# Kernel optimization log

Measured on AMD Instinct MI355X. Metric: run time of the kernel, lower is better.

## Reference

```python
import jax, jax.numpy as jnp
import numpy as np

B, C, H, W = 2, 512, 64, 64
G = 32          # GroupNorm groups
EPS = 1e-6


def setup_inputs() -> dict:
    key = jax.random.key(0)
    ks = jax.random.split(key, 10)
    s = 1.0 / np.sqrt(C)
    return {
        "x": jax.random.normal(ks[0], (B, C, H, W), dtype=jnp.float32),
        "gn_w": jnp.ones((C,), jnp.float32),
        "gn_b": jnp.zeros((C,), jnp.float32),
        "wq": jax.random.normal(ks[1], (C, C), jnp.float32) * s,
        "bq": jnp.zeros((C,), jnp.float32),
        "wk": jax.random.normal(ks[2], (C, C), jnp.float32) * s,
        "bk": jnp.zeros((C,), jnp.float32),
        "wv": jax.random.normal(ks[3], (C, C), jnp.float32) * s,
        "bv": jnp.zeros((C,), jnp.float32),
        "wo": jax.random.normal(ks[4], (C, C), jnp.float32) * s,
        "bo": jnp.zeros((C,), jnp.float32),
    }


def reference(x, gn_w, gn_b, wq, bq, wk, bk, wv, bv, wo, bo):
    b, c, h, w = x.shape
    n = h * w
    # GroupNorm(32, eps=1e-6, affine)
    xg = x.reshape(b, G, c // G, h, w)
    mu = xg.mean(axis=(2, 3, 4), keepdims=True)
    var = ((xg - mu) ** 2).mean(axis=(2, 3, 4), keepdims=True)
    hn = ((xg - mu) * jax.lax.rsqrt(var + EPS)).reshape(b, c, h, w)
    hn = hn * gn_w[None, :, None, None] + gn_b[None, :, None, None]
    # 1x1 convs == per-pixel linear over channels; tokens: b n c
    hf = hn.reshape(b, c, n)
    q = jnp.einsum('oc,bcn->bno', wq, hf) + bq  # [b, n, c]
    k = jnp.einsum('oc,bcn->bno', wk, hf) + bk
    v = jnp.einsum('oc,bcn->bno', wv, hf) + bv
    scale = jnp.asarray(c, x.dtype) ** -0.5
    att = jax.nn.softmax(jnp.einsum('bic,bjc->bij', q, k) * scale, axis=-1)
    o = jnp.einsum('bij,bjc->bic', att, v)      # [b, n, c]
    out = jnp.einsum('oc,bnc->bno', wo, o) + bo # proj_out
    return x + out.transpose(0, 2, 1).reshape(b, c, h, w)
```

## Files before the change

kernel.cpp:

```cpp
#include <hip/hip_runtime.h>
#include <hip/hip_bf16.h>


typedef float f32x4 __attribute__((ext_vector_type(4)));
typedef __bf16 bf16x8 __attribute__((ext_vector_type(8)));

typedef const __attribute__((address_space(1))) unsigned char* gas_p;
typedef __attribute__((address_space(3))) unsigned char* las_p;

__device__ __forceinline__ void gload_lds16(const void* g, void* l) {
  __builtin_amdgcn_global_load_lds((gas_p)g, (las_p)l, 16, 0, 0);
}

__global__ __launch_bounds__(256) void prelude_k(
    const float* __restrict__ wq, const float* __restrict__ wk,
    const float* __restrict__ wv, const float* __restrict__ wo,
    __hip_bfloat16* __restrict__ wqkb, __hip_bfloat16* __restrict__ wvb,
    __hip_bfloat16* __restrict__ wob, const float* __restrict__ bq,
    const float* __restrict__ bk, float* __restrict__ bqk,
    const float* __restrict__ x, float* __restrict__ stats) {
  int bid = blockIdx.x;
  if (bid < 4096) {
    const float* src;
    __hip_bfloat16* dst;
    if (bid < 1024)      { src = wq; dst = wqkb; }
    else if (bid < 2048) { src = wk; dst = wqkb + 262144; }
    else if (bid < 3072) { src = wv; dst = wvb; }
    else                 { src = wo; dst = wob; }
    int i = (bid & 1023) * 256 + threadIdx.x;
    dst[i] = __float2bfloat16(src[i]);
    return;
  }
  if (bid < 4160) {
    int bg = bid - 4096;
    const float4* p = (const float4*)(x + (size_t)bg * 65536);
    float s = 0.f, s2 = 0.f;
    for (int i = threadIdx.x; i < 16384; i += 256) {
      float4 v = p[i];
      s  += v.x + v.y + v.z + v.w;
      s2 += v.x * v.x + v.y * v.y + v.z * v.z + v.w * v.w;
    }
#pragma unroll
    for (int off = 32; off > 0; off >>= 1) {
      s  += __shfl_xor(s, off);
      s2 += __shfl_xor(s2, off);
    }
    __shared__ float rs[4], rs2[4];
    int wid = threadIdx.x >> 6, lane = threadIdx.x & 63;
    if (lane == 0) { rs[wid] = s; rs2[wid] = s2; }
    __syncthreads();
    if (threadIdx.x == 0) {
      float S  = rs[0] + rs[1] + rs[2] + rs[3];
      float S2 = rs2[0] + rs2[1] + rs2[2] + rs2[3];
      float mean = S * (1.f / 65536.f);
      float var  = S2 * (1.f / 65536.f) - mean * mean;
      stats[bg * 2]     = mean;
      stats[bg * 2 + 1] = rsqrtf(var + 1e-6f);
    }
    return;
  }
  for (int j = threadIdx.x; j < 1024; j += 256)
    bqk[j] = (j < 512) ? bq[j] : bk[j - 512];
}

__global__ __launch_bounds__(256) void gn_apply_k(const float* __restrict__ x,
                                                  const float* __restrict__ stats,
                                                  const float* __restrict__ gw,
                                                  const float* __restrict__ gb,
                                                  __hip_bfloat16* __restrict__ hf) {
  int c0 = blockIdx.x * 64, n0 = blockIdx.y * 64, b = blockIdx.z;
  __shared__ float tile[64][65];
  int tid = threadIdx.x;
  int cl = tid >> 2, q = tid & 3;
  int c = c0 + cl;
  float mean = stats[(b * 32 + (c >> 4)) * 2];
  float rstd = stats[(b * 32 + (c >> 4)) * 2 + 1];
  float sc = rstd * gw[c];
  float sh = gb[c] - mean * sc;
  const float* xr = x + ((size_t)(b * 512 + c0 + cl)) * 4096 + n0 + q * 16;
#pragma unroll
  for (int j = 0; j < 4; j++) {
    float4 v = *(const float4*)(xr + 4 * j);
    int n = q * 16 + 4 * j;
    tile[cl][n]     = v.x * sc + sh;
    tile[cl][n + 1] = v.y * sc + sh;
    tile[cl][n + 2] = v.z * sc + sh;
    tile[cl][n + 3] = v.w * sc + sh;
  }
  __syncthreads();
  int nl = tid >> 2, ch = q * 16;
  bf16x8 o0, o1;
#pragma unroll
  for (int l = 0; l < 8; l++) {
    o0[l] = (__bf16)tile[ch + l][nl];
    o1[l] = (__bf16)tile[ch + 8 + l][nl];
  }
  __hip_bfloat16* op = hf + ((size_t)(b * 4096 + n0 + nl)) * 512 + c0 + ch;
  *(uint4*)op = *(uint4*)&o0;
  *(uint4*)(op + 8) = *(uint4*)&o1;
}

__global__ __launch_bounds__(256, 4) void qkv_k(
    const __hip_bfloat16* __restrict__ hf, const __hip_bfloat16* __restrict__ wqk,
    const __hip_bfloat16* __restrict__ wv, const float* __restrict__ bqk,
    const float* __restrict__ bv, __hip_bfloat16* __restrict__ qk,
    __hip_bfloat16* __restrict__ vT) {
  bool isV = blockIdx.x >= 8;
  int m0 = isV ? (blockIdx.x - 8) * 128 : blockIdx.y * 128;
  int n0 = isV ? blockIdx.y * 128 : blockIdx.x * 128;
  const __hip_bfloat16* A  = isV ? wv : hf;
  const __hip_bfloat16* Bm = isV ? hf : wqk;

  __shared__ __align__(16) unsigned char smem[34816];
  __hip_bfloat16* As  = (__hip_bfloat16*)smem;
  __hip_bfloat16* Bs  = As + 8192;
  __hip_bfloat16* epi = (__hip_bfloat16*)smem;

  int tid  = threadIdx.x;
  int wvx  = tid >> 6, lane = tid & 63;
  int wr   = (wvx >> 1) * 64, wc = (wvx & 1) * 64;
  int quad = lane >> 4, l16 = lane & 15;

  int srow = wvx * 32 + (lane >> 2);
  int scol = (lane & 3) * 8;
  const __hip_bfloat16* gA0 = A  + (size_t)(m0 + srow) * 512 + scol;
  const __hip_bfloat16* gA1 = gA0 + (size_t)16 * 512;
  const __hip_bfloat16* gB0 = Bm + (size_t)(n0 + srow) * 512 + scol;
  const __hip_bfloat16* gB1 = gB0 + (size_t)16 * 512;

  auto stage = [&](int kk, int bsel) {
    int lb = bsel * 4096 + wvx * 1024;
    gload_lds16(gA0 + kk, &As[lb]);
    gload_lds16(gA1 + kk, &As[lb + 512]);
    gload_lds16(gB0 + kk, &Bs[lb]);
    gload_lds16(gB1 + kk, &Bs[lb + 512]);
  };

  f32x4 acc[4][4] = {};
  stage(0, 0);
  for (int kt = 0; kt < 16; kt++) {
    __syncthreads();
    if (kt + 1 < 16) stage((kt + 1) << 5, (kt + 1) & 1);
    const __hip_bfloat16* Ab = &As[(kt & 1) * 4096];
    const __hip_bfloat16* Bb = &Bs[(kt & 1) * 4096];
    bf16x8 af[4], bfr[4];
#pragma unroll
    for (int i = 0; i < 4; i++)
      af[i] = *(const bf16x8*)&Ab[(wr + i * 16 + l16) * 32 + quad * 8];
#pragma unroll
    for (int j = 0; j < 4; j++)
      bfr[j] = *(const bf16x8*)&Bb[(wc + j * 16 + l16) * 32 + quad * 8];
#pragma unroll
    for (int i = 0; i < 4; i++)
#pragma unroll
      for (int j = 0; j < 4; j++)
        acc[i][j] = __builtin_amdgcn_mfma_f32_16x16x32_bf16(af[i], bfr[j],
                                                            acc[i][j], 0, 0, 0);
  }

  float bj[4], bm[4][4];
  if (!isV) {
#pragma unroll
    for (int j = 0; j < 4; j++) bj[j] = bqk[n0 + wc + j * 16 + l16];
  } else {
#pragma unroll
    for (int i = 0; i < 4; i++)
#pragma unroll
      for (int r = 0; r < 4; r++)
        bm[i][r] = bv[m0 + wr + i * 16 + quad * 4 + r];
  }
  __syncthreads();
#pragma unroll
  for (int i = 0; i < 4; i++)
#pragma unroll
    for (int j = 0; j < 4; j++)
#pragma unroll
      for (int r = 0; r < 4; r++) {
        int ml = wr + i * 16 + quad * 4 + r;
        int nl = wc + j * 16 + l16;
        float v = acc[i][j][r] + (isV ? bm[i][r] : bj[j]);
        epi[ml * 136 + nl] = __float2bfloat16(v);
      }
  __syncthreads();
  int mr = tid >> 1, h = tid & 1;
  const __hip_bfloat16* rowp = &epi[mr * 136 + h * 64];
  if (!isV) {
    __hip_bfloat16* o = qk + (size_t)(m0 + mr) * 1024 + n0 + h * 64;
#pragma unroll
    for (int c = 0; c < 8; c++)
      *(uint4*)(o + c * 8) = *(const uint4*)(rowp + c * 8);
  } else {
    int b = (n0 + h * 64) >> 12, t = (n0 + h * 64) & 4095;
    __hip_bfloat16* o = vT + ((size_t)(b * 512 + m0 + mr)) * 4096 + t;
#pragma unroll
    for (int c = 0; c < 8; c++)
      *(uint4*)(o + c * 8) = *(const uint4*)(rowp + c * 8);
  }
}

__global__ __launch_bounds__(256, 4) void qkexp_k(
    const __hip_bfloat16* __restrict__ A, const __hip_bfloat16* __restrict__ Bm,
    __hip_bfloat16* __restrict__ Cout, float* __restrict__ psums) {
  int bx = blockIdx.x, by = blockIdx.y, bb = blockIdx.z;
  const float scale = 0.044194173824159216f;
  A  += (size_t)bb * 4096 * 1024;
  Bm += (size_t)bb * 4096 * 1024 + 512;
  size_t cbase = (size_t)bb * 4096 * 4096;
  int m0 = by * 128, n0 = bx * 128;

  __shared__ __align__(16) unsigned char smem[33792];
  __hip_bfloat16* As  = (__hip_bfloat16*)smem;
  __hip_bfloat16* Bs  = As + 8192;
  float* psum2 = (float*)(smem + 32768);

  int tid  = threadIdx.x;
  int wv   = tid >> 6, lane = tid & 63;
  int wr   = (wv >> 1) * 64, wc = (wv & 1) * 64;
  int quad = lane >> 4, l16 = lane & 15;

  int srow = wv * 32 + (lane >> 2);
  int scol = (lane & 3) * 8;
  const __hip_bfloat16* gA0 = A  + (size_t)(m0 + srow) * 1024 + scol;
  const __hip_bfloat16* gA1 = gA0 + (size_t)16 * 1024;
  const __hip_bfloat16* gB0 = Bm + (size_t)(n0 + srow) * 1024 + scol;
  const __hip_bfloat16* gB1 = gB0 + (size_t)16 * 1024;

  auto stage = [&](int kk, int bsel) {
    int lb = bsel * 4096 + wv * 1024;
    gload_lds16(gA0 + kk, &As[lb]);
    gload_lds16(gA1 + kk, &As[lb + 512]);
    gload_lds16(gB0 + kk, &Bs[lb]);
    gload_lds16(gB1 + kk, &Bs[lb + 512]);
  };

  f32x4 acc[4][4] = {};
  stage(0, 0);
  for (int kt = 0; kt < 16; kt++) {
    __syncthreads();
    if (kt + 1 < 16) stage((kt + 1) << 5, (kt + 1) & 1);
    const __hip_bfloat16* Ab = &As[(kt & 1) * 4096];
    const __hip_bfloat16* Bb = &Bs[(kt & 1) * 4096];
    bf16x8 af[4], bfr[4];
#pragma unroll
    for (int i = 0; i < 4; i++)
      af[i] = *(const bf16x8*)&Ab[(wr + i * 16 + l16) * 32 + quad * 8];
#pragma unroll
    for (int j = 0; j < 4; j++)
      bfr[j] = *(const bf16x8*)&Bb[(wc + j * 16 + l16) * 32 + quad * 8];
#pragma unroll
    for (int i = 0; i < 4; i++)
#pragma unroll
      for (int j = 0; j < 4; j++)
        acc[i][j] = __builtin_amdgcn_mfma_f32_16x16x32_bf16(af[i], bfr[j],
                                                            acc[i][j], 0, 0, 0);
  }

  float s[4][4];
#pragma unroll
  for (int i = 0; i < 4; i++)
#pragma unroll
    for (int r = 0; r < 4; r++) s[i][r] = 0.f;
#pragma unroll
  for (int i = 0; i < 4; i++)
#pragma unroll
    for (int j = 0; j < 4; j++)
#pragma unroll
      for (int r = 0; r < 4; r++) {
        int m = m0 + wr + i * 16 + quad * 4 + r;
        int n = n0 + wc + j * 16 + l16;
        float v = __expf(acc[i][j][r] * scale);
        Cout[cbase + (size_t)m * 4096 + n] = __float2bfloat16(v);
        s[i][r] += v;
      }
#pragma unroll
  for (int off = 1; off < 16; off <<= 1)
#pragma unroll
    for (int i = 0; i < 4; i++)
#pragma unroll
      for (int r = 0; r < 4; r++) s[i][r] += __shfl_xor(s[i][r], off);
  if (l16 == 0) {
#pragma unroll
    for (int i = 0; i < 4; i++)
#pragma unroll
      for (int r = 0; r < 4; r++)
        psum2[(wv & 1) * 128 + wr + i * 16 + quad * 4 + r] = s[i][r];
  }
  __syncthreads();
  if (tid < 128)
    psums[(size_t)bx * 8192 + bb * 4096 + m0 + tid] =
        psum2[tid] + psum2[128 + tid];
}

__global__ __launch_bounds__(256, 2) void pv_k(
    const __hip_bfloat16* __restrict__ P, const __hip_bfloat16* __restrict__ vT,
    __hip_bfloat16* __restrict__ part) {
  int f = blockIdx.x;
  int xcd = f & 7, s = f >> 3;
  int bx = s & 3;
  int g = xcd + 8 * (s >> 2);
  int by = g & 31, bz = g >> 5;
  int bb = bz >> 1, ks = bz & 1;
  const __hip_bfloat16* A = P  + (size_t)bb * 4096 * 4096 + (size_t)ks * 2048;
  const __hip_bfloat16* B = vT + (size_t)bb * 512 * 4096 + (size_t)ks * 2048;
  size_t cbase = (size_t)bz * 4096 * 512;
  int m0 = by * 128, n0 = bx * 128;

  __shared__ __align__(16) unsigned char smem[65536];
  __hip_bfloat16* As  = (__hip_bfloat16*)smem;
  __hip_bfloat16* Bs  = (__hip_bfloat16*)(smem + 32768);
  __hip_bfloat16* epi = (__hip_bfloat16*)smem;

  int tid = threadIdx.x, wv = tid >> 6, lane = tid & 63;
  int wr = (wv >> 1) * 64, wc = (wv & 1) * 64;
  int quad = lane >> 4, l16 = lane & 15;

  int srow = wv * 32 + (lane >> 3);
  int scol = ((lane & 7) ^ (lane >> 3)) * 8;
  const __hip_bfloat16* gA = A + (size_t)(m0 + srow) * 4096 + scol;
  const __hip_bfloat16* gB = B + (size_t)(n0 + srow) * 4096 + scol;

  auto stage = [&](int kk, int bsel) {
    __hip_bfloat16* la = &As[bsel * 8192 + wv * 2048];
    __hip_bfloat16* lb = &Bs[bsel * 8192 + wv * 2048];
#pragma unroll
    for (int c = 0; c < 4; c++) {
      gload_lds16(gA + kk + (size_t)(c * 8) * 4096, la + c * 512);
      gload_lds16(gB + kk + (size_t)(c * 8) * 4096, lb + c * 512);
    }
  };

  f32x4 acc[4][4] = {};
  stage(0, 0);
  for (int kt = 0; kt < 32; kt++) {
    __syncthreads();
    if (kt + 1 < 32) stage((kt + 1) << 6, (kt + 1) & 1);
    const __hip_bfloat16* Ab = &As[(kt & 1) * 8192];
    const __hip_bfloat16* Bb = &Bs[(kt & 1) * 8192];
#pragma unroll
    for (int ksub = 0; ksub < 2; ksub++) {
      bf16x8 af[4], bfr[4];
#pragma unroll
      for (int i = 0; i < 4; i++) {
        int r = wr + i * 16 + l16;
        af[i] = *(const bf16x8*)&Ab[r * 64 + ((ksub * 4 + quad) ^ (r & 7)) * 8];
      }
#pragma unroll
      for (int j = 0; j < 4; j++) {
        int r = wc + j * 16 + l16;
        bfr[j] = *(const bf16x8*)&Bb[r * 64 + ((ksub * 4 + quad) ^ (r & 7)) * 8];
      }
#pragma unroll
      for (int i = 0; i < 4; i++)
#pragma unroll
        for (int j = 0; j < 4; j++)
          acc[i][j] = __builtin_amdgcn_mfma_f32_16x16x32_bf16(af[i], bfr[j],
                                                              acc[i][j], 0, 0, 0);
    }
  }

  __syncthreads();
#pragma unroll
  for (int i = 0; i < 4; i++)
#pragma unroll
    for (int j = 0; j < 4; j++)
#pragma unroll
      for (int r = 0; r < 4; r++)
        epi[(wr + i * 16 + quad * 4 + r) * 136 + wc + j * 16 + l16] =
            __float2bfloat16(acc[i][j][r]);
  __syncthreads();
  int mr = tid >> 1, h = tid & 1;
  const __hip_bfloat16* rowp = &epi[mr * 136 + h * 64];
  __hip_bfloat16* o = part + cbase + (size_t)(m0 + mr) * 512 + n0 + h * 64;
#pragma unroll
  for (int c = 0; c < 8; c++)
    *(uint4*)(o + c * 8) = *(const uint4*)(rowp + c * 8);
}

__global__ __launch_bounds__(256) void reduce_k(
    const __hip_bfloat16* __restrict__ part, const float* __restrict__ psums,
    __hip_bfloat16* __restrict__ obuf) {
  size_t i8 = (size_t)blockIdx.x * 256 + threadIdx.x;
  size_t perb = (size_t)4096 * 512 / 8;
  size_t b = i8 / perb, r = i8 - b * perb;
  int t = (int)(r >> 6);
  int lane = threadIdx.x & 63;
  float ps = psums[(size_t)(lane & 31) * 8192 + b * 4096 + t];
#pragma unroll
  for (int off = 1; off < 32; off <<= 1) ps += __shfl_xor(ps, off);
  float inv = 1.f / ps;
  float acc[8] = {};
#pragma unroll
  for (int ks = 0; ks < 2; ks++) {
    bf16x8 v = ((const bf16x8*)part)[(b * 2 + ks) * perb + r];
#pragma unroll
    for (int l = 0; l < 8; l++) acc[l] += (float)v[l];
  }
  bf16x8 o;
#pragma unroll
  for (int l = 0; l < 8; l++) o[l] = (__bf16)(acc[l] * inv);
  ((bf16x8*)obuf)[b * perb + r] = o;
}

__global__ __launch_bounds__(256, 2) void oproj_k(
    const __hip_bfloat16* __restrict__ Wo, const __hip_bfloat16* __restrict__ O,
    float* __restrict__ out, const float* __restrict__ bias,
    const float* __restrict__ resid) {
  int m0 = blockIdx.y * 64, n0 = blockIdx.x * 128, bb = blockIdx.z;
  O += (size_t)bb * 4096 * 512;
  size_t cbase = (size_t)bb * 512 * 4096;

  __shared__ __align__(16) unsigned char smem[24576];
  __hip_bfloat16* As  = (__hip_bfloat16*)smem;
  __hip_bfloat16* Bs  = As + 4096;
  __hip_bfloat16* epi = (__hip_bfloat16*)smem;

  int tid = threadIdx.x, wv = tid >> 6, lane = tid & 63;
  int wr = (wv >> 1) * 32, wc = (wv & 1) * 64;
  int quad = lane >> 4, l16 = lane & 15;

  int lr = lane >> 2, scol = (lane & 3) * 8;
  const __hip_bfloat16* gA  = Wo + (size_t)(m0 + wv * 16 + lr) * 512 + scol;
  const __hip_bfloat16* gB0 = O  + (size_t)(n0 + wv * 32 + lr) * 512 + scol;
  const __hip_bfloat16* gB1 = gB0 + (size_t)16 * 512;

  auto stage = [&](int kk, int bsel) {
    gload_lds16(gA + kk, &As[bsel * 2048 + wv * 512]);
    gload_lds16(gB0 + kk, &Bs[bsel * 4096 + wv * 1024]);
    gload_lds16(gB1 + kk, &Bs[bsel * 4096 + wv * 1024 + 512]);
  };

  f32x4 acc[2][4] = {};
  stage(0, 0);
  for (int kt = 0; kt < 16; kt++) {
    __syncthreads();
    if (kt + 1 < 16) stage((kt + 1) << 5, (kt + 1) & 1);
    const __hip_bfloat16* Ab = &As[(kt & 1) * 2048];
    const __hip_bfloat16* Bb = &Bs[(kt & 1) * 4096];
    bf16x8 af[2], bfr[4];
#pragma unroll
    for (int i = 0; i < 2; i++)
      af[i] = *(const bf16x8*)&Ab[(wr + i * 16 + l16) * 32 + quad * 8];
#pragma unroll
    for (int j = 0; j < 4; j++)
      bfr[j] = *(const bf16x8*)&Bb[(wc + j * 16 + l16) * 32 + quad * 8];
#pragma unroll
    for (int i = 0; i < 2; i++)
#pragma unroll
      for (int j = 0; j < 4; j++)
        acc[i][j] = __builtin_amdgcn_mfma_f32_16x16x32_bf16(af[i], bfr[j],
                                                            acc[i][j], 0, 0, 0);
  }

  float pre[2][4];
#pragma unroll
  for (int i = 0; i < 2; i++)
#pragma unroll
    for (int r = 0; r < 4; r++)
      pre[i][r] = bias[m0 + wr + i * 16 + quad * 4 + r];
  __syncthreads();
#pragma unroll
  for (int i = 0; i < 2; i++)
#pragma unroll
    for (int j = 0; j < 4; j++)
#pragma unroll
      for (int r = 0; r < 4; r++)
        epi[(wr + i * 16 + quad * 4 + r) * 136 + wc + j * 16 + l16] =
            __float2bfloat16(acc[i][j][r] + pre[i][r]);
  __syncthreads();
  int mr = tid >> 2, seg = tid & 3;
  const __hip_bfloat16* rowp = &epi[mr * 136 + seg * 32];
  size_t obase = cbase + (size_t)(m0 + mr) * 4096 + n0 + seg * 32;
#pragma unroll
  for (int c = 0; c < 4; c++) {
    bf16x8 val = *(const bf16x8*)(rowp + c * 8);
    size_t idx = obase + c * 8;
    float4 r0 = *(const float4*)&resid[idx];
    float4 r1 = *(const float4*)&resid[idx + 4];
    float4 o0, o1;
    o0.x = r0.x + (float)val[0]; o0.y = r0.y + (float)val[1];
    o0.z = r0.z + (float)val[2]; o0.w = r0.w + (float)val[3];
    o1.x = r1.x + (float)val[4]; o1.y = r1.y + (float)val[5];
    o1.z = r1.z + (float)val[6]; o1.w = r1.w + (float)val[7];
    *(float4*)&out[idx] = o0;
    *(float4*)&out[idx + 4] = o1;
  }
}

extern "C" void kernel_launch(void* const* d_in, const int* in_sizes, int n_in,
                              void* d_out, int out_size, void* d_ws,
                              size_t ws_size, hipStream_t stream) {
  const float* xp  = (const float*)d_in[0];
  const float* gwp = (const float*)d_in[1];
  const float* gbp = (const float*)d_in[2];
  const float* wqp = (const float*)d_in[3];
  const float* bqp = (const float*)d_in[4];
  const float* wkp = (const float*)d_in[5];
  const float* bkp = (const float*)d_in[6];
  const float* wvp = (const float*)d_in[7];
  const float* bvp = (const float*)d_in[8];
  const float* wop = (const float*)d_in[9];
  const float* bop = (const float*)d_in[10];
  float* outp = (float*)d_out;

  char* w = (char*)d_ws;
  size_t off = 0;
  auto alloc = [&](size_t bytes) {
    void* p = w + off;
    off += (bytes + 255) & ~(size_t)255;
    return p;
  };
  float* stats         = (float*)alloc(64 * 2 * sizeof(float));
  __hip_bfloat16* hf   = (__hip_bfloat16*)alloc((size_t)2 * 4096 * 512 * 2);
  __hip_bfloat16* wqkb = (__hip_bfloat16*)alloc((size_t)1024 * 512 * 2);
  __hip_bfloat16* wvb  = (__hip_bfloat16*)alloc((size_t)512 * 512 * 2);
  __hip_bfloat16* wob  = (__hip_bfloat16*)alloc((size_t)512 * 512 * 2);
  float* bqk           = (float*)alloc(1024 * sizeof(float));
  float* psums         = (float*)alloc((size_t)32 * 8192 * sizeof(float));
  __hip_bfloat16* qk   = (__hip_bfloat16*)alloc((size_t)2 * 4096 * 1024 * 2);
  __hip_bfloat16* vT   = (__hip_bfloat16*)alloc((size_t)2 * 512 * 4096 * 2);
  __hip_bfloat16* obuf = (__hip_bfloat16*)alloc((size_t)2 * 4096 * 512 * 2);
  __hip_bfloat16* part = (__hip_bfloat16*)alloc((size_t)4 * 4096 * 512 * 2);
  __hip_bfloat16* Sbuf = (__hip_bfloat16*)alloc((size_t)2 * 4096 * 4096 * 2);

  prelude_k<<<4161, 256, 0, stream>>>(wqp, wkp, wvp, wop, wqkb, wvb, wob,
                                      bqp, bkp, bqk, xp, stats);

  gn_apply_k<<<dim3(8, 64, 2), 256, 0, stream>>>(xp, stats, gwp, gbp, hf);

  qkv_k<<<dim3(12, 64, 1), 256, 0, stream>>>(hf, wqkb, wvb, bqk, bvp, qk, vT);

  qkexp_k<<<dim3(32, 32, 2), 256, 0, stream>>>(qk, qk, Sbuf, psums);

  pv_k<<<512, 256, 0, stream>>>(Sbuf, vT, part);

  reduce_k<<<2048, 256, 0, stream>>>(part, psums, obuf);

  oproj_k<<<dim3(32, 8, 2), 256, 0, stream>>>(wob, obuf, outp, bop, xp);
}
```

Baseline: 266.1 us.

## Fuse QK^T exp and PV into a flash-style attention kernel

Replaces the separate QK^T+exp kernel, which wrote a full 4096x4096 bf16 score matrix per batch, and the PV GEMM that read it back, with a single attention kernel. Each block keeps a 64-query tile, computes exp(scores) for 128-key chunks into LDS and multiplies them with V immediately, with the key range split in two halves. This removes the large score-buffer round trip through HBM. In exchange it launches only 256 blocks of 512 threads with about 130KB of LDS each, so occupancy and parallelism are lower. Softmax is still unshifted exp, as before.

```diff
diff --git a/kernel.cpp b/kernel.cpp
--- a/kernel.cpp
+++ b/kernel.cpp
@@ -198,206 +198,170 @@
   }
 }
 
-__global__ __launch_bounds__(256, 4) void qkexp_k(
-    const __hip_bfloat16* __restrict__ A, const __hip_bfloat16* __restrict__ Bm,
-    __hip_bfloat16* __restrict__ Cout, float* __restrict__ psums) {
-  int bx = blockIdx.x, by = blockIdx.y, bb = blockIdx.z;
+__global__ __launch_bounds__(512, 2) void attn_k(
+    const __hip_bfloat16* __restrict__ qk, const __hip_bfloat16* __restrict__ vT,
+    __hip_bfloat16* __restrict__ part, float* __restrict__ rsum) {
   const float scale = 0.044194173824159216f;
-  A  += (size_t)bb * 4096 * 1024;
-  Bm += (size_t)bb * 4096 * 1024 + 512;
-  size_t cbase = (size_t)bb * 4096 * 4096;
-  int m0 = by * 128, n0 = bx * 128;
-
-  __shared__ __align__(16) unsigned char smem[33792];
-  __hip_bfloat16* As  = (__hip_bfloat16*)smem;
-  __hip_bfloat16* Bs  = As + 8192;
-  float* psum2 = (float*)(smem + 32768);
-
-  int tid  = threadIdx.x;
-  int wv   = tid >> 6, lane = tid & 63;
-  int wr   = (wv >> 1) * 64, wc = (wv & 1) * 64;
+  int bid = blockIdx.x;
+  int g2 = bid & 7;
+  int b = g2 >> 2, spl = (g2 >> 1) & 1;
+  int qtile = (g2 & 1) * 32 + (bid >> 3);
+
+  const __hip_bfloat16* qkb = qk + (size_t)b * 4194304;
+  const __hip_bfloat16* vTb = vT + (size_t)b * 2097152;
+
+  __shared__ __align__(16) unsigned char smem[133120];
+  __hip_bfloat16* Qs = (__hip_bfloat16*)smem;
+  __hip_bfloat16* Ks = (__hip_bfloat16*)(smem + 16384);
+  __hip_bfloat16* Vs = (__hip_bfloat16*)(smem + 49152);
+  __hip_bfloat16* Ps = (__hip_bfloat16*)(smem + 114688);
+  float* Rs = (float*)(smem + 132096);
+
+  int tid = threadIdx.x, wv = tid >> 6, lane = tid & 63;
   int quad = lane >> 4, l16 = lane & 15;
-
-  int srow = wv * 32 + (lane >> 2);
-  int scol = (lane & 3) * 8;
-  const __hip_bfloat16* gA0 = A  + (size_t)(m0 + srow) * 1024 + scol;
-  const __hip_bfloat16* gA1 = gA0 + (size_t)16 * 1024;
-  const __hip_bfloat16* gB0 = Bm + (size_t)(n0 + srow) * 1024 + scol;
-  const __hip_bfloat16* gB1 = gB0 + (size_t)16 * 1024;
-
-  auto stage = [&](int kk, int bsel) {
-    int lb = bsel * 4096 + wv * 1024;
-    gload_lds16(gA0 + kk, &As[lb]);
-    gload_lds16(gA1 + kk, &As[lb + 512]);
-    gload_lds16(gB0 + kk, &Bs[lb]);
-    gload_lds16(gB1 + kk, &Bs[lb + 512]);
+  int q0 = (wv >> 2) * 32;
+  int kvc0 = (wv & 3) * 32;
+  int wd0 = (wv & 3) * 128;
+
+  int srow8 = lane >> 3;
+  int schk = ((lane & 7) ^ srow8) * 8;
+  const __hip_bfloat16* gQ = qkb + (size_t)(qtile * 64 + wv * 8 + srow8) * 1024 + schk;
+  const __hip_bfloat16* gK0 =
+      qkb + (size_t)(spl * 2048 + wv * 16 + srow8) * 1024 + 512 + schk;
+  const __hip_bfloat16* gK1 = gK0 + (size_t)8 * 1024;
+  const __hip_bfloat16* gV = vTb + (size_t)(wv * 64 + (lane >> 2)) * 4096 +
+                             spl * 2048 + (lane & 3) * 8;
+
+  auto stageQK = [&](int t, int s, int bsel) {
+    int koff = t * 131072 + s * 64;
+    gload_lds16(gQ + s * 64, &Qs[bsel * 4096 + wv * 512]);
+    gload_lds16(gK0 + koff, &Ks[bsel * 8192 + wv * 1024]);
+    gload_lds16(gK1 + koff, &Ks[bsel * 8192 + wv * 1024 + 512]);
   };
-
-  f32x4 acc[4][4] = {};
-  stage(0, 0);
-  for (int kt = 0; kt < 16; kt++) {
-    __syncthreads();
-    if (kt + 1 < 16) stage((kt + 1) << 5, (kt + 1) & 1);
-    const __hip_bfloat16* Ab = &As[(kt & 1) * 4096];
-    const __hip_bfloat16* Bb = &Bs[(kt & 1) * 4096];
-    bf16x8 af[4], bfr[4];
-#pragma unroll
-    for (int i = 0; i < 4; i++)
-      af[i] = *(const bf16x8*)&Ab[(wr + i * 16 + l16) * 32 + quad * 8];
-#pragma unroll
-    for (int j = 0; j < 4; j++)
-      bfr[j] = *(const bf16x8*)&Bb[(wc + j * 16 + l16) * 32 + quad * 8];
-#pragma unroll
-    for (int i = 0; i < 4; i++)
-#pragma unroll
-      for (int j = 0; j < 4; j++)
-        acc[i][j] = __builtin_amdgcn_mfma_f32_16x16x32_bf16(af[i], bfr[j],
-                                                            acc[i][j], 0, 0, 0);
-  }
-
-  float s[4][4];
-#pragma unroll
-  for (int i = 0; i < 4; i++)
-#pragma unroll
-    for (int r = 0; r < 4; r++) s[i][r] = 0.f;
-#pragma unroll
-  for (int i = 0; i < 4; i++)
-#pragma unroll
-    for (int j = 0; j < 4; j++)
-#pragma unroll
-      for (int r = 0; r < 4; r++) {
-        int m = m0 + wr + i * 16 + quad * 4 + r;
-        int n = n0 + wc + j * 16 + l16;
-        float v = __expf(acc[i][j][r] * scale);
-        Cout[cbase + (size_t)m * 4096 + n] = __float2bfloat16(v);
-        s[i][r] += v;
+  auto stageV = [&](int t, int sub, int vb) {
+    const __hip_bfloat16* g = gV + t * 128 + sub * 32;
+#pragma unroll
+    for (int c = 0; c < 4; c++)
+      gload_lds16(g + (size_t)(c * 16) * 4096, &Vs[vb * 16384 + wv * 2048 + c * 512]);
+  };
+
+  f32x4 accS[2][2] = {};
+  f32x4 accO[8][2] = {};
+  float rsr[8] = {};
+
+  stageQK(0, 0, 0);
+  for (int t = 0; t < 16; t++) {
+    for (int s = 0; s < 8; s++) {
+      __syncthreads();
+      if (s < 7) stageQK(t, s + 1, (s + 1) & 1);
+      else stageV(t, 0, 0);
+      const __hip_bfloat16* Qb = &Qs[(s & 1) * 4096];
+      const __hip_bfloat16* Kb = &Ks[(s & 1) * 8192];
+      bf16x8 aq[2][2], bkf[2][2];
+#pragma unroll
+      for (int ii = 0; ii < 2; ii++)
+#pragma unroll
+        for (int kk = 0; kk < 2; kk++) {
+          int r = q0 + ii * 16 + l16;
+          aq[ii][kk] = *(const bf16x8*)&Qb[r * 64 + ((kk * 4 + quad) ^ (r & 7)) * 8];
+        }
+#pragma unroll
+      for (int jj = 0; jj < 2; jj++)
+#pragma unroll
+        for (int kk = 0; kk < 2; kk++) {
+          int r = kvc0 + jj * 16 + l16;
+          bkf[jj][kk] = *(const bf16x8*)&Kb[r * 64 + ((kk * 4 + quad) ^ (r & 7)) * 8];
+        }
+#pragma unroll
+      for (int ii = 0; ii < 2; ii++)
+#pragma unroll
+        for (int jj = 0; jj < 2; jj++)
+#pragma unroll
+          for (int kk = 0; kk < 2; kk++)
+            accS[ii][jj] = __builtin_amdgcn_mfma_f32_16x16x32_bf16(
+                aq[ii][kk], bkf[jj][kk], accS[ii][jj], 0, 0, 0);
+    }
+#pragma unroll
+    for (int ii = 0; ii < 2; ii++)
+#pragma unroll
+      for (int jj = 0; jj < 2; jj++) {
+#pragma unroll
+        for (int rr = 0; rr < 4; rr++) {
+          float p = __expf(accS[ii][jj][rr] * scale);
+          rsr[ii * 4 + rr] += p;
+          Ps[(q0 + ii * 16 + quad * 4 + rr) * 136 + kvc0 + jj * 16 + l16] =
+              __float2bfloat16(p);
+        }
+        accS[ii][jj] = (f32x4){0.f, 0.f, 0.f, 0.f};
       }
-#pragma unroll
-  for (int off = 1; off < 16; off <<= 1)
-#pragma unroll
-    for (int i = 0; i < 4; i++)
-#pragma unroll
-      for (int r = 0; r < 4; r++) s[i][r] += __shfl_xor(s[i][r], off);
+    for (int sub = 0; sub < 4; sub++) {
+      __syncthreads();
+      if (sub < 3) stageV(t, sub + 1, (sub + 1) & 1);
+      else if (t + 1 < 16) stageQK(t + 1, 0, 0);
+      const __hip_bfloat16* Vb = &Vs[(sub & 1) * 16384];
+      bf16x8 pa[2], bvf[8];
+#pragma unroll
+      for (int ii = 0; ii < 2; ii++) {
+        int r = q0 + ii * 16 + l16;
+        pa[ii] = *(const bf16x8*)&Ps[r * 136 + sub * 32 + quad * 8];
+      }
+#pragma unroll
+      for (int jj = 0; jj < 8; jj++) {
+        int r = wd0 + jj * 16 + l16;
+        bvf[jj] = *(const bf16x8*)&Vb[r * 32 + quad * 8];
+      }
+#pragma unroll
+      for (int jj = 0; jj < 8; jj++)
+#pragma unroll
+        for (int ii = 0; ii < 2; ii++)
+          accO[jj][ii] = __builtin_amdgcn_mfma_f32_16x16x32_bf16(
+              pa[ii], bvf[jj], accO[jj][ii], 0, 0, 0);
+    }
+  }
+
+  size_t pbase = ((size_t)(spl * 2 + b) * 4096 + qtile * 64) * 512;
+#pragma unroll
+  for (int ii = 0; ii < 2; ii++)
+#pragma unroll
+    for (int rr = 0; rr < 4; rr++) {
+      int row = q0 + ii * 16 + quad * 4 + rr;
+#pragma unroll
+      for (int jj = 0; jj < 8; jj++)
+        part[pbase + (size_t)row * 512 + wd0 + jj * 16 + l16] =
+            __float2bfloat16(accO[jj][ii][rr]);
+    }
+#pragma unroll
+  for (int k = 0; k < 8; k++)
+#pragma unroll
+    for (int off = 1; off < 16; off <<= 1) rsr[k] += __shfl_xor(rsr[k], off);
   if (l16 == 0) {
 #pragma unroll
-    for (int i = 0; i < 4; i++)
-#pragma unroll
-      for (int r = 0; r < 4; r++)
-        psum2[(wv & 1) * 128 + wr + i * 16 + quad * 4 + r] = s[i][r];
+    for (int ii = 0; ii < 2; ii++)
+#pragma unroll
+      for (int rr = 0; rr < 4; rr++)
+        Rs[(wv & 3) * 64 + q0 + ii * 16 + quad * 4 + rr] = rsr[ii * 4 + rr];
   }
   __syncthreads();
-  if (tid < 128)
-    psums[(size_t)bx * 8192 + bb * 4096 + m0 + tid] =
-        psum2[tid] + psum2[128 + tid];
-}
-
-__global__ __launch_bounds__(256, 2) void pv_k(
-    const __hip_bfloat16* __restrict__ P, const __hip_bfloat16* __restrict__ vT,
-    __hip_bfloat16* __restrict__ part) {
-  int f = blockIdx.x;
-  int xcd = f & 7, s = f >> 3;
-  int bx = s & 3;
-  int g = xcd + 8 * (s >> 2);
-  int by = g & 31, bz = g >> 5;
-  int bb = bz >> 1, ks = bz & 1;
-  const __hip_bfloat16* A = P  + (size_t)bb * 4096 * 4096 + (size_t)ks * 2048;
-  const __hip_bfloat16* B = vT + (size_t)bb * 512 * 4096 + (size_t)ks * 2048;
-  size_t cbase = (size_t)bz * 4096 * 512;
-  int m0 = by * 128, n0 = bx * 128;
-
-  __shared__ __align__(16) unsigned char smem[65536];
-  __hip_bfloat16* As  = (__hip_bfloat16*)smem;
-  __hip_bfloat16* Bs  = (__hip_bfloat16*)(smem + 32768);
-  __hip_bfloat16* epi = (__hip_bfloat16*)smem;
-
-  int tid = threadIdx.x, wv = tid >> 6, lane = tid & 63;
-  int wr = (wv >> 1) * 64, wc = (wv & 1) * 64;
-  int quad = lane >> 4, l16 = lane & 15;
-
-  int srow = wv * 32 + (lane >> 3);
-  int scol = ((lane & 7) ^ (lane >> 3)) * 8;
-  const __hip_bfloat16* gA = A + (size_t)(m0 + srow) * 4096 + scol;
-  const __hip_bfloat16* gB = B + (size_t)(n0 + srow) * 4096 + scol;
-
-  auto stage = [&](int kk, int bsel) {
-    __hip_bfloat16* la = &As[bsel * 8192 + wv * 2048];
-    __hip_bfloat16* lb = &Bs[bsel * 8192 + wv * 2048];
-#pragma unroll
-    for (int c = 0; c < 4; c++) {
-      gload_lds16(gA + kk + (size_t)(c * 8) * 4096, la + c * 512);
-      gload_lds16(gB + kk + (size_t)(c * 8) * 4096, lb + c * 512);
-    }
-  };
-
-  f32x4 acc[4][4] = {};
-  stage(0, 0);
-  for (int kt = 0; kt < 32; kt++) {
-    __syncthreads();
-    if (kt + 1 < 32) stage((kt + 1) << 6, (kt + 1) & 1);
-    const __hip_bfloat16* Ab = &As[(kt & 1) * 8192];
-    const __hip_bfloat16* Bb = &Bs[(kt & 1) * 8192];
-#pragma unroll
-    for (int ksub = 0; ksub < 2; ksub++) {
-      bf16x8 af[4], bfr[4];
-#pragma unroll
-      for (int i = 0; i < 4; i++) {
-        int r = wr + i * 16 + l16;
-        af[i] = *(const bf16x8*)&Ab[r * 64 + ((ksub * 4 + quad) ^ (r & 7)) * 8];
-      }
-#pragma unroll
-      for (int j = 0; j < 4; j++) {
-        int r = wc + j * 16 + l16;
-        bfr[j] = *(const bf16x8*)&Bb[r * 64 + ((ksub * 4 + quad) ^ (r & 7)) * 8];
-      }
-#pragma unroll
-      for (int i = 0; i < 4; i++)
-#pragma unroll
-        for (int j = 0; j < 4; j++)
-          acc[i][j] = __builtin_amdgcn_mfma_f32_16x16x32_bf16(af[i], bfr[j],
-                                                              acc[i][j], 0, 0, 0);
-    }
-  }
-
-  __syncthreads();
-#pragma unroll
-  for (int i = 0; i < 4; i++)
-#pragma unroll
-    for (int j = 0; j < 4; j++)
-#pragma unroll
-      for (int r = 0; r < 4; r++)
-        epi[(wr + i * 16 + quad * 4 + r) * 136 + wc + j * 16 + l16] =
-            __float2bfloat16(acc[i][j][r]);
-  __syncthreads();
-  int mr = tid >> 1, h = tid & 1;
-  const __hip_bfloat16* rowp = &epi[mr * 136 + h * 64];
-  __hip_bfloat16* o = part + cbase + (size_t)(m0 + mr) * 512 + n0 + h * 64;
-#pragma unroll
-  for (int c = 0; c < 8; c++)
-    *(uint4*)(o + c * 8) = *(const uint4*)(rowp + c * 8);
-}
-
-__global__ __launch_bounds__(256) void reduce_k(
-    const __hip_bfloat16* __restrict__ part, const float* __restrict__ psums,
+  if (tid < 64)
+    rsum[spl * 8192 + b * 4096 + qtile * 64 + tid] =
+        Rs[tid] + Rs[64 + tid] + Rs[128 + tid] + Rs[192 + tid];
+}
+
+__global__ __launch_bounds__(256) void reduce2_k(
+    const __hip_bfloat16* __restrict__ part, const float* __restrict__ rsum,
     __hip_bfloat16* __restrict__ obuf) {
   size_t i8 = (size_t)blockIdx.x * 256 + threadIdx.x;
-  size_t perb = (size_t)4096 * 512 / 8;
+  size_t perb = 262144;
   size_t b = i8 / perb, r = i8 - b * perb;
   int t = (int)(r >> 6);
-  int lane = threadIdx.x & 63;
-  float ps = psums[(size_t)(lane & 31) * 8192 + b * 4096 + t];
-#pragma unroll
-  for (int off = 1; off < 32; off <<= 1) ps += __shfl_xor(ps, off);
+  float ps = rsum[b * 4096 + t] + rsum[8192 + b * 4096 + t];
   float inv = 1.f / ps;
-  float acc[8] = {};
-#pragma unroll
-  for (int ks = 0; ks < 2; ks++) {
-    bf16x8 v = ((const bf16x8*)part)[(b * 2 + ks) * perb + r];
-#pragma unroll
-    for (int l = 0; l < 8; l++) acc[l] += (float)v[l];
-  }
+  bf16x8 v0 = ((const bf16x8*)part)[b * perb + r];
+  bf16x8 v1 = ((const bf16x8*)part)[(2 + b) * perb + r];
   bf16x8 o;
 #pragma unroll
-  for (int l = 0; l < 8; l++) o[l] = (__bf16)(acc[l] * inv);
+  for (int l = 0; l < 8; l++)
+    o[l] = (__bf16)(((float)v0[l] + (float)v1[l]) * inv);
   ((bf16x8*)obuf)[b * perb + r] = o;
 }
 
@@ -515,12 +479,11 @@
   __hip_bfloat16* wvb  = (__hip_bfloat16*)alloc((size_t)512 * 512 * 2);
   __hip_bfloat16* wob  = (__hip_bfloat16*)alloc((size_t)512 * 512 * 2);
   float* bqk           = (float*)alloc(1024 * sizeof(float));
-  float* psums         = (float*)alloc((size_t)32 * 8192 * sizeof(float));
+  float* rsum          = (float*)alloc((size_t)2 * 2 * 4096 * sizeof(float));
   __hip_bfloat16* qk   = (__hip_bfloat16*)alloc((size_t)2 * 4096 * 1024 * 2);
   __hip_bfloat16* vT   = (__hip_bfloat16*)alloc((size_t)2 * 512 * 4096 * 2);
   __hip_bfloat16* obuf = (__hip_bfloat16*)alloc((size_t)2 * 4096 * 512 * 2);
   __hip_bfloat16* part = (__hip_bfloat16*)alloc((size_t)4 * 4096 * 512 * 2);
-  __hip_bfloat16* Sbuf = (__hip_bfloat16*)alloc((size_t)2 * 4096 * 4096 * 2);
 
   prelude_k<<<4161, 256, 0, stream>>>(wqp, wkp, wvp, wop, wqkb, wvb, wob,
                                       bqp, bkp, bqk, xp, stats);
@@ -529,11 +492,9 @@
 
   qkv_k<<<dim3(12, 64, 1), 256, 0, stream>>>(hf, wqkb, wvb, bqk, bvp, qk, vT);
 
-  qkexp_k<<<dim3(32, 32, 2), 256, 0, stream>>>(qk, qk, Sbuf, psums);
-
-  pv_k<<<512, 256, 0, stream>>>(Sbuf, vT, part);
-
-  reduce_k<<<2048, 256, 0, stream>>>(part, psums, obuf);
+  attn_k<<<256, 512, 0, stream>>>(qk, vT, part, rsum);
+
+  reduce2_k<<<2048, 256, 0, stream>>>(part, rsum, obuf);
 
   oproj_k<<<dim3(32, 8, 2), 256, 0, stream>>>(wob, obuf, outp, bop, xp);
 }
```

Result: slower. 282.8 us (+6.3%).

## Drop split-K in PV GEMM and fuse softmax normalization into its epilogue

Applied to the files above, without the earlier changes.

The PV GEMM changes from 128x128 tiles with a two-way split-K to 64x128 tiles covering the full K=4096, keeping the grid at 512 blocks. Each block now sums the per-row softmax partial sums itself and scales the accumulators by the reciprocal before writing bf16 output straight to obuf. This removes the separate reduce kernel, the partial-result buffer and its write/read traffic, and one launch. The cost is a smaller M tile, so each block reloads more V per unit of work and runs a K loop twice as long.

```diff
diff --git a/kernel.cpp b/kernel.cpp
--- a/kernel.cpp
+++ b/kernel.cpp
@@ -292,113 +292,99 @@
 }
 
 __global__ __launch_bounds__(256, 2) void pv_k(
-    const __hip_bfloat16* __restrict__ P, const __hip_bfloat16* __restrict__ vT,
-    __hip_bfloat16* __restrict__ part) {
+    const __hip_bfloat16* __restrict__ S, const __hip_bfloat16* __restrict__ vT,
+    const float* __restrict__ psums, __hip_bfloat16* __restrict__ obuf) {
   int f = blockIdx.x;
-  int xcd = f & 7, s = f >> 3;
-  int bx = s & 3;
-  int g = xcd + 8 * (s >> 2);
-  int by = g & 31, bz = g >> 5;
-  int bb = bz >> 1, ks = bz & 1;
-  const __hip_bfloat16* A = P  + (size_t)bb * 4096 * 4096 + (size_t)ks * 2048;
-  const __hip_bfloat16* B = vT + (size_t)bb * 512 * 4096 + (size_t)ks * 2048;
-  size_t cbase = (size_t)bz * 4096 * 512;
-  int m0 = by * 128, n0 = bx * 128;
-
-  __shared__ __align__(16) unsigned char smem[65536];
+  int xcd = f & 7, sidx = f >> 3;
+  int bx = sidx & 3;
+  int g = xcd + 8 * (sidx >> 2);
+  int by = g & 63, b = g >> 6;
+  int m0 = by * 64, n0 = bx * 128;
+  const __hip_bfloat16* A  = S  + (size_t)b * 4096 * 4096;
+  const __hip_bfloat16* Bv = vT + (size_t)b * 512 * 4096;
+
+  __shared__ __align__(16) unsigned char smem[49664];
   __hip_bfloat16* As  = (__hip_bfloat16*)smem;
-  __hip_bfloat16* Bs  = (__hip_bfloat16*)(smem + 32768);
+  __hip_bfloat16* Bs  = (__hip_bfloat16*)(smem + 16384);
   __hip_bfloat16* epi = (__hip_bfloat16*)smem;
+  float* inv = (float*)(smem + 49152);
 
   int tid = threadIdx.x, wv = tid >> 6, lane = tid & 63;
-  int wr = (wv >> 1) * 64, wc = (wv & 1) * 64;
+  int wr = (wv >> 1) * 32, wc = (wv & 1) * 64;
   int quad = lane >> 4, l16 = lane & 15;
 
-  int srow = wv * 32 + (lane >> 3);
-  int scol = ((lane & 7) ^ (lane >> 3)) * 8;
-  const __hip_bfloat16* gA = A + (size_t)(m0 + srow) * 4096 + scol;
-  const __hip_bfloat16* gB = B + (size_t)(n0 + srow) * 4096 + scol;
+  int srow8 = lane >> 3;
+  int schk = ((lane & 7) ^ srow8) * 8;
+  const __hip_bfloat16* gA0 = A  + (size_t)(m0 + wv * 8 + srow8) * 4096 + schk;
+  const __hip_bfloat16* gA1 = gA0 + (size_t)32 * 4096;
+  const __hip_bfloat16* gB0 = Bv + (size_t)(n0 + wv * 8 + srow8) * 4096 + schk;
 
   auto stage = [&](int kk, int bsel) {
-    __hip_bfloat16* la = &As[bsel * 8192 + wv * 2048];
-    __hip_bfloat16* lb = &Bs[bsel * 8192 + wv * 2048];
-#pragma unroll
-    for (int c = 0; c < 4; c++) {
-      gload_lds16(gA + kk + (size_t)(c * 8) * 4096, la + c * 512);
-      gload_lds16(gB + kk + (size_t)(c * 8) * 4096, lb + c * 512);
-    }
+    gload_lds16(gA0 + kk, &As[bsel * 4096 + wv * 512]);
+    gload_lds16(gA1 + kk, &As[bsel * 4096 + wv * 512 + 2048]);
+#pragma unroll
+    for (int r = 0; r < 4; r++)
+      gload_lds16(gB0 + kk + (size_t)(r * 32) * 4096,
+                  &Bs[bsel * 8192 + wv * 512 + r * 2048]);
   };
 
-  f32x4 acc[4][4] = {};
+  f32x4 acc[2][4] = {};
   stage(0, 0);
-  for (int kt = 0; kt < 32; kt++) {
+  if (tid < 64) {
+    float ssum = 0.f;
+#pragma unroll
+    for (int j = 0; j < 32; j++)
+      ssum += psums[(size_t)j * 8192 + b * 4096 + m0 + tid];
+    inv[tid] = 1.f / ssum;
+  }
+  for (int kt = 0; kt < 64; kt++) {
     __syncthreads();
-    if (kt + 1 < 32) stage((kt + 1) << 6, (kt + 1) & 1);
-    const __hip_bfloat16* Ab = &As[(kt & 1) * 8192];
+    if (kt + 1 < 64) stage((kt + 1) << 6, (kt + 1) & 1);
+    const __hip_bfloat16* Ab = &As[(kt & 1) * 4096];
     const __hip_bfloat16* Bb = &Bs[(kt & 1) * 8192];
 #pragma unroll
-    for (int ksub = 0; ksub < 2; ksub++) {
-      bf16x8 af[4], bfr[4];
-#pragma unroll
-      for (int i = 0; i < 4; i++) {
+    for (int kk = 0; kk < 2; kk++) {
+      bf16x8 af[2], bfr[4];
+#pragma unroll
+      for (int i = 0; i < 2; i++) {
         int r = wr + i * 16 + l16;
-        af[i] = *(const bf16x8*)&Ab[r * 64 + ((ksub * 4 + quad) ^ (r & 7)) * 8];
+        af[i] = *(const bf16x8*)&Ab[r * 64 + (((kk * 4 + quad) ^ (r & 7)) << 3)];
       }
 #pragma unroll
       for (int j = 0; j < 4; j++) {
         int r = wc + j * 16 + l16;
-        bfr[j] = *(const bf16x8*)&Bb[r * 64 + ((ksub * 4 + quad) ^ (r & 7)) * 8];
+        bfr[j] = *(const bf16x8*)&Bb[r * 64 + (((kk * 4 + quad) ^ (r & 7)) << 3)];
       }
 #pragma unroll
-      for (int i = 0; i < 4; i++)
+      for (int i = 0; i < 2; i++)
 #pragma unroll
         for (int j = 0; j < 4; j++)
           acc[i][j] = __builtin_amdgcn_mfma_f32_16x16x32_bf16(af[i], bfr[j],
                                                               acc[i][j], 0, 0, 0);
     }
   }
-
-  __syncthreads();
-#pragma unroll
-  for (int i = 0; i < 4; i++)
+  float iv[2][4];
+#pragma unroll
+  for (int i = 0; i < 2; i++)
+#pragma unroll
+    for (int r = 0; r < 4; r++) iv[i][r] = inv[wr + i * 16 + quad * 4 + r];
+  __syncthreads();
+#pragma unroll
+  for (int i = 0; i < 2; i++)
 #pragma unroll
     for (int j = 0; j < 4; j++)
 #pragma unroll
       for (int r = 0; r < 4; r++)
         epi[(wr + i * 16 + quad * 4 + r) * 136 + wc + j * 16 + l16] =
-            __float2bfloat16(acc[i][j][r]);
-  __syncthreads();
-  int mr = tid >> 1, h = tid & 1;
-  const __hip_bfloat16* rowp = &epi[mr * 136 + h * 64];
-  __hip_bfloat16* o = part + cbase + (size_t)(m0 + mr) * 512 + n0 + h * 64;
-#pragma unroll
-  for (int c = 0; c < 8; c++)
+            __float2bfloat16(acc[i][j][r] * iv[i][r]);
+  __syncthreads();
+  int mr = tid >> 2, seg = tid & 3;
+  const __hip_bfloat16* rowp = &epi[mr * 136 + seg * 32];
+  __hip_bfloat16* o =
+      obuf + ((size_t)(b * 4096 + m0 + mr)) * 512 + n0 + seg * 32;
+#pragma unroll
+  for (int c = 0; c < 4; c++)
     *(uint4*)(o + c * 8) = *(const uint4*)(rowp + c * 8);
-}
-
-__global__ __launch_bounds__(256) void reduce_k(
-    const __hip_bfloat16* __restrict__ part, const float* __restrict__ psums,
-    __hip_bfloat16* __restrict__ obuf) {
-  size_t i8 = (size_t)blockIdx.x * 256 + threadIdx.x;
-  size_t perb = (size_t)4096 * 512 / 8;
-  size_t b = i8 / perb, r = i8 - b * perb;
-  int t = (int)(r >> 6);
-  int lane = threadIdx.x & 63;
-  float ps = psums[(size_t)(lane & 31) * 8192 + b * 4096 + t];
-#pragma unroll
-  for (int off = 1; off < 32; off <<= 1) ps += __shfl_xor(ps, off);
-  float inv = 1.f / ps;
-  float acc[8] = {};
-#pragma unroll
-  for (int ks = 0; ks < 2; ks++) {
-    bf16x8 v = ((const bf16x8*)part)[(b * 2 + ks) * perb + r];
-#pragma unroll
-    for (int l = 0; l < 8; l++) acc[l] += (float)v[l];
-  }
-  bf16x8 o;
-#pragma unroll
-  for (int l = 0; l < 8; l++) o[l] = (__bf16)(acc[l] * inv);
-  ((bf16x8*)obuf)[b * perb + r] = o;
 }
 
 __global__ __launch_bounds__(256, 2) void oproj_k(
@@ -519,7 +505,6 @@
   __hip_bfloat16* qk   = (__hip_bfloat16*)alloc((size_t)2 * 4096 * 1024 * 2);
   __hip_bfloat16* vT   = (__hip_bfloat16*)alloc((size_t)2 * 512 * 4096 * 2);
   __hip_bfloat16* obuf = (__hip_bfloat16*)alloc((size_t)2 * 4096 * 512 * 2);
-  __hip_bfloat16* part = (__hip_bfloat16*)alloc((size_t)4 * 4096 * 512 * 2);
   __hip_bfloat16* Sbuf = (__hip_bfloat16*)alloc((size_t)2 * 4096 * 4096 * 2);
 
   prelude_k<<<4161, 256, 0, stream>>>(wqp, wkp, wvp, wop, wqkb, wvb, wob,
@@ -531,9 +516,7 @@
 
   qkexp_k<<<dim3(32, 32, 2), 256, 0, stream>>>(qk, qk, Sbuf, psums);
 
-  pv_k<<<512, 256, 0, stream>>>(Sbuf, vT, part);
-
-  reduce_k<<<2048, 256, 0, stream>>>(part, psums, obuf);
+  pv_k<<<512, 256, 0, stream>>>(Sbuf, vT, psums, obuf);
 
   oproj_k<<<dim3(32, 8, 2), 256, 0, stream>>>(wob, obuf, outp, bop, xp);
 }
```

Result: faster. 257.7 us (median of 2 runs) (-3.2%).
